# Kernel tuning notes

Measured on AMD Instinct MI355X. Metric: run time of the kernel, lower is better.

## Reference

```python
import jax, jax.numpy as jnp
import numpy as np

NUM_AUTHOR = 16604
NUM_PAPER = 12455
NUM_NODES = NUM_AUTHOR + NUM_PAPER  # 29059
EMBED_DIM = 300
B = 32768          # batch of query nodes
E = 1048576        # total neighbor edges (avg degree 32)


def setup_inputs() -> dict:
    key = jax.random.key(0)
    k1, k2, k3, k4, k5, k6 = jax.random.split(key, 6)
    nodes = jax.random.randint(k1, (B,), 0, NUM_NODES)
    seg = jnp.sort(jax.random.randint(k2, (E,), 0, B))
    neighbors = jax.random.randint(k3, (E,), 0, NUM_NODES)
    embeddings = jax.random.normal(k4, (NUM_NODES, EMBED_DIM), dtype=jnp.float32)
    # linear1: Linear(3*300 -> 300)
    lim = 1.0 / np.sqrt(3 * EMBED_DIM)
    W1 = jax.random.uniform(k5, (EMBED_DIM, 3 * EMBED_DIM), dtype=jnp.float32, minval=-lim, maxval=lim)
    b1 = jax.random.uniform(k6, (EMBED_DIM,), dtype=jnp.float32, minval=-lim, maxval=lim)
    return {"nodes": nodes, "seg": seg, "neighbors": neighbors,
            "embeddings": embeddings, "W1": W1, "b1": b1}


def reference(nodes, seg, neighbors, embeddings, W1, b1):
    # Gather neighbor embeddings: [E, D] (dominant memory traffic)
    nb_emb = embeddings[neighbors]
    # type_1 = same node type as the query node, type_2 = the other type
    same = (neighbors < NUM_AUTHOR) == (nodes[seg] < NUM_AUTHOR)  # [E] bool
    w1 = same.astype(nb_emb.dtype)[:, None]
    w2 = 1.0 - w1
    sum1 = jax.ops.segment_sum(nb_emb * w1, seg, num_segments=B)   # [B, D]
    sum2 = jax.ops.segment_sum(nb_emb * w2, seg, num_segments=B)
    cnt1 = jax.ops.segment_sum(w1[:, 0], seg, num_segments=B)[:, None]  # [B,1]
    cnt2 = jax.ops.segment_sum(w2[:, 0], seg, num_segments=B)[:, None]
    # mean pooling; empty type falls back to ones (as in the torch code)
    t1 = jnp.where(cnt1 > 0, sum1 / jnp.maximum(cnt1, 1.0), 1.0)
    t2 = jnp.where(cnt2 > 0, sum2 / jnp.maximum(cnt2, 1.0), 1.0)
    self_f = embeddings[nodes]  # [B, D]
    combined = jnp.concatenate([self_f, t1, t2], axis=-1)  # [B, 3D]
    return combined @ W1.T + b1  # [B, D]
```

## Files before the change

kernel.cpp:

```cpp
#include <hip/hip_runtime.h>
#include <hip/hip_bf16.h>

#define NUM_AUTHOR 16604
#define EMB_D      300
#define BQ         32768
#define NEDGE      1048576
#define KPAD 960
#define NPAD 320
#define DPAD 320
#define NNODES 29059

#define SEG_BLOCKS 4096
#define PW_BLOCKS  1200
#define CE_BLOCKS  4541

typedef __attribute__((ext_vector_type(8))) short bf16x8;
typedef __attribute__((ext_vector_type(4))) float f32x4;

__device__ __forceinline__ unsigned short f2bf(float f) {
  unsigned int u = __float_as_uint(f);
  u += 0x7fffu + ((u >> 16) & 1u);
  return (unsigned short)(u >> 16);
}

__device__ __forceinline__ void async_copy16(const void* g, void* lds_base) {
  __builtin_amdgcn_global_load_lds(
      (const __attribute__((address_space(1))) unsigned int*)g,
      (__attribute__((address_space(3))) unsigned int*)lds_base, 16, 0, 0);
}

__global__ void prep_all(const int* __restrict__ seg, int* __restrict__ start,
                         const float* __restrict__ W1, unsigned short* __restrict__ Wt,
                         const float* __restrict__ emb, unsigned short* __restrict__ embB) {
  int blk = blockIdx.x;
  if (blk < SEG_BLOCKS) {
    int i = blk * 256 + threadIdx.x;
    int s = seg[i];
    int prev = (i == 0) ? -1 : seg[i - 1];
    if (s != prev) {
      for (int b = prev + 1; b <= s; ++b) start[b] = i;
    }
    if (i == NEDGE - 1) {
      for (int b = s + 1; b <= BQ; ++b) start[b] = NEDGE;
    }
  } else if (blk < SEG_BLOCKS + PW_BLOCKS) {
    int i = (blk - SEG_BLOCKS) * 256 + threadIdx.x;
    int n = i / KPAD, k = i % KPAD;
    int sec = k / 320, kk = k % 320;
    unsigned short v = 0;
    if (n < 300 && kk < 300) v = f2bf(W1[n * 900 + sec * 300 + kk]);
    Wt[i] = v;
  } else {
    int i = (blk - SEG_BLOCKS - PW_BLOCKS) * 256 + threadIdx.x;
    if (i >= NNODES * 40) return;
    int r = i / 40, q = i % 40;
    const float* src = emb + (size_t)r * EMB_D + q * 8;
    unsigned int u[4] = {0, 0, 0, 0};
    if (q < 37) {
      float4 v0 = *(const float4*)src;
      float4 v1 = *(const float4*)(src + 4);
      u[0] = (unsigned int)f2bf(v0.x) | ((unsigned int)f2bf(v0.y) << 16);
      u[1] = (unsigned int)f2bf(v0.z) | ((unsigned int)f2bf(v0.w) << 16);
      u[2] = (unsigned int)f2bf(v1.x) | ((unsigned int)f2bf(v1.y) << 16);
      u[3] = (unsigned int)f2bf(v1.z) | ((unsigned int)f2bf(v1.w) << 16);
    } else if (q == 37) {
      float4 v0 = *(const float4*)src;
      u[0] = (unsigned int)f2bf(v0.x) | ((unsigned int)f2bf(v0.y) << 16);
      u[1] = (unsigned int)f2bf(v0.z) | ((unsigned int)f2bf(v0.w) << 16);
    }
    ((uint4*)embB)[i] = (uint4){u[0], u[1], u[2], u[3]};
  }
}

__device__ __forceinline__ void accum8(uint4 p, int bit,
                                       float2* atot, float2* a1) {
  unsigned int pk[4] = {p.x, p.y, p.z, p.w};
  float2 v[4];
  #pragma unroll
  for (int k = 0; k < 4; ++k) {
    v[k].x = __uint_as_float(pk[k] << 16);
    v[k].y = __uint_as_float(pk[k] & 0xffff0000u);
  }
  #pragma unroll
  for (int k = 0; k < 4; ++k) {
    atot[k].x += v[k].x; atot[k].y += v[k].y;
  }
  if (__builtin_amdgcn_readfirstlane(bit)) {
    #pragma unroll
    for (int k = 0; k < 4; ++k) {
      a1[k].x += v[k].x; a1[k].y += v[k].y;
    }
  }
}

__global__ __launch_bounds__(128) void pool(
    const int* __restrict__ nodes, const int* __restrict__ neighbors,
    const int* __restrict__ start, const unsigned short* __restrict__ embB,
    unsigned short* __restrict__ comb) {
  int b = blockIdx.x * 2 + (threadIdx.x >> 6);
  int l = threadIdx.x & 63;
  int s0 = start[b], s1 = start[b + 1];
  int node = nodes[b];
  int qa = (node < NUM_AUTHOR) ? 1 : 0;
  bool act = (l < 40);
  const unsigned short* ep = embB + 8 * l;

  float2 atot[4], a1[4];
  #pragma unroll
  for (int k = 0; k < 4; ++k) {
    atot[k] = make_float2(0.f, 0.f);
    a1[k]   = make_float2(0.f, 0.f);
  }
  int c1 = 0;
  int rem = s1 - s0;

  for (int base = 0; base < rem; base += 64) {
    int cl = min(64, rem - base);
    int idx = neighbors[s0 + base + min(l, cl - 1)];
    int same = (((idx < NUM_AUTHOR) ? 1 : 0) == qa) ? 1 : 0;
    unsigned long long bal = __ballot(same != 0);
    unsigned long long msk = (cl >= 64) ? ~0ull : ((1ull << cl) - 1ull);
    c1 += __popcll(bal & msk);
    int off = idx * DPAD;

    int j2 = 0;
    for (; j2 + 8 <= cl; j2 += 8) {
      int o[8];
      #pragma unroll
      for (int q = 0; q < 8; ++q) o[q] = __shfl(off, j2 + q);
      if (act) {
        uint4 p[8];
        #pragma unroll
        for (int q = 0; q < 8; ++q) p[q] = *(const uint4*)(ep + o[q]);
        #pragma unroll
        for (int q = 0; q < 8; ++q)
          accum8(p[q], (int)((bal >> (j2 + q)) & 1), atot, a1);
      }
    }
    for (; j2 < cl; ++j2) {
      int o = __shfl(off, j2);
      if (act) {
        uint4 p = *(const uint4*)(ep + o);
        accum8(p, (int)((bal >> j2) & 1), atot, a1);
      }
    }
  }

  int c2 = rem - c1;
  if (!act) return;

  uint4 selfv = *(const uint4*)(embB + (size_t)node * DPAD + 8 * l);
  float r1 = c1 ? 1.0f / (float)c1 : 0.0f;
  float r2 = c2 ? 1.0f / (float)c2 : 0.0f;
  unsigned int o1[4], o2[4];
  #pragma unroll
  for (int k = 0; k < 4; ++k) {
    float t1lo = c1 ? a1[k].x * r1 : 1.0f;
    float t1hi = c1 ? a1[k].y * r1 : 1.0f;
    float t2lo = c2 ? (atot[k].x - a1[k].x) * r2 : 1.0f;
    float t2hi = c2 ? (atot[k].y - a1[k].y) * r2 : 1.0f;
    o1[k] = (unsigned int)f2bf(t1lo) | ((unsigned int)f2bf(t1hi) << 16);
    o2[k] = (unsigned int)f2bf(t2lo) | ((unsigned int)f2bf(t2hi) << 16);
  }
  uint4* crow = (uint4*)(comb + (size_t)b * KPAD);
  crow[l]      = selfv;
  crow[40 + l] = (uint4){o1[0], o1[1], o1[2], o1[3]};
  crow[80 + l] = (uint4){o2[0], o2[1], o2[2], o2[3]};
}

__global__ __launch_bounds__(256) void gemm(
    const unsigned short* __restrict__ A,
    const unsigned short* __restrict__ Bt,
    const float* __restrict__ b1,
    float* __restrict__ out) {
  __shared__ __align__(16) unsigned short As[2][64 * 64];
  __shared__ __align__(16) unsigned short Bs[2][160 * 64];

  int tid  = threadIdx.x;
  int lane = tid & 63;
  int w    = tid >> 6;
  int quad = lane >> 4;
  int l16  = lane & 15;
  int bm = blockIdx.x >> 1;
  int bn = blockIdx.x & 1;
  int wm = w >> 1, wn = w & 1;

  f32x4 acc[2][5];
  for (int i = 0; i < 2; ++i)
    for (int j = 0; j < 5; ++j)
      acc[i][j] = (f32x4){0.f, 0.f, 0.f, 0.f};

  const size_t Abase = (size_t)bm * 64 * KPAD;
  const size_t Bbase = (size_t)bn * 160 * KPAD;

  auto stage = [&](int kt, int buf) {
    int k0 = kt * 64;
    for (int c = w; c < 8; c += 4) {
      int flat = c * 64 + lane;
      int row = flat >> 3, g = flat & 7;
      int kq = g ^ (row & 7);
      const unsigned short* gp = A + Abase + (size_t)row * KPAD + k0 + kq * 8;
      async_copy16(gp, (char*)&As[buf][0] + c * 1024);
    }
    for (int c = w; c < 20; c += 4) {
      int flat = c * 64 + lane;
      int row = flat >> 3, g = flat & 7;
      int kq = g ^ (row & 7);
      const unsigned short* gp = Bt + Bbase + (size_t)row * KPAD + k0 + kq * 8;
      async_copy16(gp, (char*)&Bs[buf][0] + c * 1024);
    }
  };

  stage(0, 0);
  for (int kt = 0; kt < KPAD / 64; ++kt) {
    int cur = kt & 1;
    __syncthreads();
    if (kt + 1 < KPAD / 64) stage(kt + 1, cur ^ 1);
    #pragma unroll
    for (int ks = 0; ks < 2; ++ks) {
      int gi = ks * 4 + quad;
      bf16x8 af[2], bf[5];
      #pragma unroll
      for (int rt = 0; rt < 2; ++rt) {
        int row = wm * 32 + rt * 16 + l16;
        af[rt] = *(const bf16x8*)&As[cur][row * 64 + ((gi ^ (row & 7)) << 3)];
      }
      #pragma unroll
      for (int ct = 0; ct < 5; ++ct) {
        int row = wn * 80 + ct * 16 + l16;
        bf[ct] = *(const bf16x8*)&Bs[cur][row * 64 + ((gi ^ (row & 7)) << 3)];
      }
      #pragma unroll
      for (int rt = 0; rt < 2; ++rt)
        #pragma unroll
        for (int ct = 0; ct < 5; ++ct)
          acc[rt][ct] = __builtin_amdgcn_mfma_f32_16x16x32_bf16(
              af[rt], bf[ct], acc[rt][ct], 0, 0, 0);
    }
  }

  int m0 = bm * 64 + wm * 32;
  int n0 = bn * 160 + wn * 80;
  for (int ct = 0; ct < 5; ++ct) {
    int n = n0 + ct * 16 + l16;
    if (n >= 300) continue;
    float bias = b1[n];
    for (int rt = 0; rt < 2; ++rt) {
      int m = m0 + rt * 16 + quad * 4;
      for (int r = 0; r < 4; ++r)
        out[(size_t)(m + r) * 300 + n] = acc[rt][ct][r] + bias;
    }
  }
}

__global__ __launch_bounds__(128) void pool_f32(
    const int* __restrict__ nodes, const int* __restrict__ neighbors,
    const int* __restrict__ start, const float* __restrict__ emb,
    unsigned short* __restrict__ comb) {
  int b = blockIdx.x;
  int t = threadIdx.x;
  if (t >= 80) return;
  int s0 = start[b], s1 = start[b + 1];
  int node = nodes[b];
  int qa = (node < NUM_AUTHOR) ? 1 : 0;
  bool act = (t < 75);
  float a1x = 0.f, a1y = 0.f, a1z = 0.f, a1w = 0.f;
  float a2x = 0.f, a2y = 0.f, a2z = 0.f, a2w = 0.f;
  int c1 = 0;
  #pragma unroll 2
  for (int j = s0; j < s1; ++j) {
    int nb = neighbors[j];
    int fl = (((nb < NUM_AUTHOR) ? 1 : 0) == qa) ? 1 : 0;
    c1 += fl;
    if (act) {
      const float4 v = *(const float4*)(emb + (size_t)nb * EMB_D + 4 * t);
      float w = fl ? 1.0f : 0.0f;
      float u = 1.0f - w;
      a1x += w * v.x; a1y += w * v.y; a1z += w * v.z; a1w += w * v.w;
      a2x += u * v.x; a2y += u * v.y; a2z += u * v.z; a2w += u * v.w;
    }
  }
  int c2 = (s1 - s0) - c1;
  unsigned int ps0 = 0, ps1 = 0, p10 = 0, p11 = 0, p20 = 0, p21 = 0;
  if (act) {
    const float4 sv = *(const float4*)(emb + (size_t)node * EMB_D + 4 * t);
    float r1 = c1 ? 1.0f / (float)c1 : 0.0f;
    float r2 = c2 ? 1.0f / (float)c2 : 0.0f;
    float t1x = c1 ? a1x * r1 : 1.0f, t1y = c1 ? a1y * r1 : 1.0f;
    float t1z = c1 ? a1z * r1 : 1.0f, t1w = c1 ? a1w * r1 : 1.0f;
    float t2x = c2 ? a2x * r2 : 1.0f, t2y = c2 ? a2y * r2 : 1.0f;
    float t2z = c2 ? a2z * r2 : 1.0f, t2w = c2 ? a2w * r2 : 1.0f;
    ps0 = (unsigned int)f2bf(sv.x) | ((unsigned int)f2bf(sv.y) << 16);
    ps1 = (unsigned int)f2bf(sv.z) | ((unsigned int)f2bf(sv.w) << 16);
    p10 = (unsigned int)f2bf(t1x) | ((unsigned int)f2bf(t1y) << 16);
    p11 = (unsigned int)f2bf(t1z) | ((unsigned int)f2bf(t1w) << 16);
    p20 = (unsigned int)f2bf(t2x) | ((unsigned int)f2bf(t2y) << 16);
    p21 = (unsigned int)f2bf(t2z) | ((unsigned int)f2bf(t2w) << 16);
  }
  unsigned int* crow = (unsigned int*)(comb + (size_t)b * KPAD);
  crow[2 * t]       = ps0;  crow[2 * t + 1]       = ps1;
  crow[160 + 2 * t] = p10;  crow[160 + 2 * t + 1] = p11;
  crow[320 + 2 * t] = p20;  crow[320 + 2 * t + 1] = p21;
}

__global__ void seg_bounds_only(const int* __restrict__ seg, int* __restrict__ start) {
  int i = blockIdx.x * 256 + threadIdx.x;
  if (i >= NEDGE) return;
  int s = seg[i];
  int prev = (i == 0) ? -1 : seg[i - 1];
  if (s != prev) for (int b = prev + 1; b <= s; ++b) start[b] = i;
  if (i == NEDGE - 1) for (int b = s + 1; b <= BQ; ++b) start[b] = NEDGE;
}
__global__ void prep_w_only(const float* __restrict__ W1, unsigned short* __restrict__ Wt) {
  int i = blockIdx.x * 256 + threadIdx.x;
  if (i >= NPAD * KPAD) return;
  int n = i / KPAD, k = i % KPAD;
  int sec = k / 320, kk = k % 320;
  unsigned short v = 0;
  if (n < 300 && kk < 300) v = f2bf(W1[n * 900 + sec * 300 + kk]);
  Wt[i] = v;
}

extern "C" void kernel_launch(void* const* d_in, const int* in_sizes, int n_in,
                              void* d_out, int out_size, void* d_ws, size_t ws_size,
                              hipStream_t stream) {
  const int* nodes     = (const int*)d_in[0];
  const int* seg       = (const int*)d_in[1];
  const int* neighbors = (const int*)d_in[2];
  const float* emb     = (const float*)d_in[3];
  const float* W1      = (const float*)d_in[4];
  const float* b1      = (const float*)d_in[5];
  float* out           = (float*)d_out;

  char* ws = (char*)d_ws;
  int* start           = (int*)ws;
  unsigned short* Wt   = (unsigned short*)(ws + 131584);
  unsigned short* comb = (unsigned short*)(ws + 746496);
  unsigned short* embB = (unsigned short*)(ws + 63661056);
  const size_t WS_NEEDED = 82258816;

  if (ws_size >= WS_NEEDED) {
    prep_all<<<SEG_BLOCKS + PW_BLOCKS + CE_BLOCKS, 256, 0, stream>>>(
        seg, start, W1, Wt, emb, embB);
    pool<<<BQ / 2, 128, 0, stream>>>(nodes, neighbors, start, embB, comb);
  } else {
    seg_bounds_only<<<SEG_BLOCKS, 256, 0, stream>>>(seg, start);
    prep_w_only<<<PW_BLOCKS, 256, 0, stream>>>(W1, Wt);
    pool_f32<<<BQ, 128, 0, stream>>>(nodes, neighbors, start, emb, comb);
  }
  gemm<<<1024, 256, 0, stream>>>(comb, Wt, b1, out);
}
```

Before: 227.2 us.

## Software-pipeline neighbor gathers in pool and enlarge GEMM tile to 128 rows

The pool kernel now reads neighbor indices straight from memory per lane, in groups of eight, and double-buffers the embedding gathers so the loads for the next group are issued while the current group is accumulated. This replaces the per-chunk ballot/shuffle scheme and adds an occupancy hint. The GEMM now uses a 128-row M tile in dynamic LDS with a swizzled block order for L2 locality, keeping the old kernel as a fallback. In exchange it uses more registers and more LDS per block, which lowers occupancy.

```diff
diff --git a/kernel.cpp b/kernel.cpp
--- a/kernel.cpp
+++ b/kernel.cpp
@@ -93,17 +93,20 @@
   }
 }
 
-__global__ __launch_bounds__(128) void pool(
+__global__ __launch_bounds__(128, 4) void pool(
     const int* __restrict__ nodes, const int* __restrict__ neighbors,
     const int* __restrict__ start, const unsigned short* __restrict__ embB,
     unsigned short* __restrict__ comb) {
   int b = blockIdx.x * 2 + (threadIdx.x >> 6);
   int l = threadIdx.x & 63;
-  int s0 = start[b], s1 = start[b + 1];
   int node = nodes[b];
   int qa = (node < NUM_AUTHOR) ? 1 : 0;
   bool act = (l < 40);
-  const unsigned short* ep = embB + 8 * l;
+
+  int s0u  = __builtin_amdgcn_readfirstlane(start[b]);
+  int remu = __builtin_amdgcn_readfirstlane(start[b + 1]) - s0u;
+  int qau  = __builtin_amdgcn_readfirstlane(qa);
+  const int* nb = neighbors + s0u;
 
   float2 atot[4], a1[4];
   #pragma unroll
@@ -112,41 +115,53 @@
     a1[k]   = make_float2(0.f, 0.f);
   }
   int c1 = 0;
-  int rem = s1 - s0;
-
-  for (int base = 0; base < rem; base += 64) {
-    int cl = min(64, rem - base);
-    int idx = neighbors[s0 + base + min(l, cl - 1)];
-    int same = (((idx < NUM_AUTHOR) ? 1 : 0) == qa) ? 1 : 0;
-    unsigned long long bal = __ballot(same != 0);
-    unsigned long long msk = (cl >= 64) ? ~0ull : ((1ull << cl) - 1ull);
-    c1 += __popcll(bal & msk);
-    int off = idx * DPAD;
-
-    int j2 = 0;
-    for (; j2 + 8 <= cl; j2 += 8) {
-      int o[8];
-      #pragma unroll
-      for (int q = 0; q < 8; ++q) o[q] = __shfl(off, j2 + q);
-      if (act) {
-        uint4 p[8];
-        #pragma unroll
-        for (int q = 0; q < 8; ++q) p[q] = *(const uint4*)(ep + o[q]);
-        #pragma unroll
-        for (int q = 0; q < 8; ++q)
-          accum8(p[q], (int)((bal >> (j2 + q)) & 1), atot, a1);
-      }
-    }
-    for (; j2 < cl; ++j2) {
-      int o = __shfl(off, j2);
-      if (act) {
-        uint4 p = *(const uint4*)(ep + o);
-        accum8(p, (int)((bal >> j2) & 1), atot, a1);
-      }
-    }
-  }
-
-  int c2 = rem - c1;
+
+  auto loadg = [&](uint4* p, int* bt, int g) {
+    #pragma unroll
+    for (int q = 0; q < 8; ++q) {
+      int ii = nb[g * 8 + q];
+      bt[q] = ((((ii < NUM_AUTHOR) ? 1 : 0) == qau) ? 1 : 0);
+      const unsigned short* rp = embB + (size_t)ii * DPAD;
+      if (act) p[q] = *(const uint4*)(rp + 8 * l);
+    }
+  };
+  auto accg = [&](const uint4* p, const int* bt) {
+    #pragma unroll
+    for (int q = 0; q < 8; ++q) {
+      c1 += bt[q];
+      if (act) accum8(p[q], bt[q], atot, a1);
+    }
+  };
+
+  int ng = remu >> 3;
+  if (ng > 0) {
+    uint4 pA[8], pB[8];
+    int bA[8], bB[8];
+    loadg(pA, bA, 0);
+    int g = 1;
+    for (; g + 1 < ng; g += 2) {
+      loadg(pB, bB, g);     accg(pA, bA);
+      loadg(pA, bA, g + 1); accg(pB, bB);
+    }
+    if (g < ng) {
+      loadg(pB, bB, g);     accg(pA, bA);
+      accg(pB, bB);
+    } else {
+      accg(pA, bA);
+    }
+  }
+  for (int j = ng * 8; j < remu; ++j) {
+    int ii = nb[j];
+    int bt = ((((ii < NUM_AUTHOR) ? 1 : 0) == qau) ? 1 : 0);
+    c1 += bt;
+    if (act) {
+      const unsigned short* rp = embB + (size_t)ii * DPAD;
+      uint4 p = *(const uint4*)(rp + 8 * l);
+      accum8(p, bt, atot, a1);
+    }
+  }
+
+  int c2 = remu - c1;
   if (!act) return;
 
   uint4 selfv = *(const uint4*)(embB + (size_t)node * DPAD + 8 * l);
@@ -173,6 +188,98 @@
     const unsigned short* __restrict__ Bt,
     const float* __restrict__ b1,
     float* __restrict__ out) {
+  extern __shared__ unsigned short lds[];
+  unsigned short* As = lds;
+  unsigned short* Bs = lds + 2 * 8192;
+
+  int tid  = threadIdx.x;
+  int lane = tid & 63;
+  int w    = tid >> 6;
+  int quad = lane >> 4;
+  int l16  = lane & 15;
+  int P = blockIdx.x;
+  int L = (P & 7) * 64 + (P >> 3);
+  int bm = L >> 1;
+  int bn = L & 1;
+  int wm = w >> 1, wn = w & 1;
+
+  f32x4 acc[4][5];
+  #pragma unroll
+  for (int i = 0; i < 4; ++i)
+    #pragma unroll
+    for (int j = 0; j < 5; ++j)
+      acc[i][j] = (f32x4){0.f, 0.f, 0.f, 0.f};
+
+  const size_t Abase = (size_t)bm * 128 * KPAD;
+  const size_t Bbase = (size_t)bn * 160 * KPAD;
+
+  auto stage = [&](int kt, int buf) {
+    int k0 = kt * 64;
+    char* Ad = (char*)(As + buf * 8192);
+    char* Bd = (char*)(Bs + buf * 10240);
+    for (int c = w; c < 16; c += 4) {
+      int flat = c * 64 + lane;
+      int row = flat >> 3, g = flat & 7;
+      int kq = g ^ (row & 7);
+      async_copy16(A + Abase + (size_t)row * KPAD + k0 + kq * 8, Ad + c * 1024);
+    }
+    for (int c = w; c < 20; c += 4) {
+      int flat = c * 64 + lane;
+      int row = flat >> 3, g = flat & 7;
+      int kq = g ^ (row & 7);
+      async_copy16(Bt + Bbase + (size_t)row * KPAD + k0 + kq * 8, Bd + c * 1024);
+    }
+  };
+
+  stage(0, 0);
+  for (int kt = 0; kt < KPAD / 64; ++kt) {
+    int cur = kt & 1;
+    __syncthreads();
+    if (kt + 1 < KPAD / 64) stage(kt + 1, cur ^ 1);
+    const unsigned short* Ac = As + cur * 8192;
+    const unsigned short* Bc = Bs + cur * 10240;
+    #pragma unroll
+    for (int ks = 0; ks < 2; ++ks) {
+      int gi = ks * 4 + quad;
+      bf16x8 af[4], bfr[5];
+      #pragma unroll
+      for (int rt = 0; rt < 4; ++rt) {
+        int row = wm * 64 + rt * 16 + l16;
+        af[rt] = *(const bf16x8*)&Ac[row * 64 + ((gi ^ (row & 7)) << 3)];
+      }
+      #pragma unroll
+      for (int ct = 0; ct < 5; ++ct) {
+        int row = wn * 80 + ct * 16 + l16;
+        bfr[ct] = *(const bf16x8*)&Bc[row * 64 + ((gi ^ (row & 7)) << 3)];
+      }
+      #pragma unroll
+      for (int rt = 0; rt < 4; ++rt)
+        #pragma unroll
+        for (int ct = 0; ct < 5; ++ct)
+          acc[rt][ct] = __builtin_amdgcn_mfma_f32_16x16x32_bf16(
+              af[rt], bfr[ct], acc[rt][ct], 0, 0, 0);
+    }
+  }
+
+  int m0 = bm * 128 + wm * 64;
+  int n0 = bn * 160 + wn * 80;
+  for (int ct = 0; ct < 5; ++ct) {
+    int n = n0 + ct * 16 + l16;
+    if (n >= 300) continue;
+    float bias = b1[n];
+    for (int rt = 0; rt < 4; ++rt) {
+      int m = m0 + rt * 16 + quad * 4;
+      for (int r = 0; r < 4; ++r)
+        out[(size_t)(m + r) * 300 + n] = acc[rt][ct][r] + bias;
+    }
+  }
+}
+
+__global__ __launch_bounds__(256) void gemm_fb(
+    const unsigned short* __restrict__ A,
+    const unsigned short* __restrict__ Bt,
+    const float* __restrict__ b1,
+    float* __restrict__ out) {
   __shared__ __align__(16) unsigned short As[2][64 * 64];
   __shared__ __align__(16) unsigned short Bs[2][160 * 64];
 
@@ -219,7 +326,7 @@
     #pragma unroll
     for (int ks = 0; ks < 2; ++ks) {
       int gi = ks * 4 + quad;
-      bf16x8 af[2], bf[5];
+      bf16x8 af[2], bfr[5];
       #pragma unroll
       for (int rt = 0; rt < 2; ++rt) {
         int row = wm * 32 + rt * 16 + l16;
@@ -228,14 +335,14 @@
       #pragma unroll
       for (int ct = 0; ct < 5; ++ct) {
         int row = wn * 80 + ct * 16 + l16;
-        bf[ct] = *(const bf16x8*)&Bs[cur][row * 64 + ((gi ^ (row & 7)) << 3)];
+        bfr[ct] = *(const bf16x8*)&Bs[cur][row * 64 + ((gi ^ (row & 7)) << 3)];
       }
       #pragma unroll
       for (int rt = 0; rt < 2; ++rt)
         #pragma unroll
         for (int ct = 0; ct < 5; ++ct)
           acc[rt][ct] = __builtin_amdgcn_mfma_f32_16x16x32_bf16(
-              af[rt], bf[ct], acc[rt][ct], 0, 0, 0);
+              af[rt], bfr[ct], acc[rt][ct], 0, 0, 0);
     }
   }
 
@@ -339,6 +446,14 @@
   unsigned short* embB = (unsigned short*)(ws + 63661056);
   const size_t WS_NEEDED = 82258816;
 
+  static int big_lds_ok = -1;
+  if (big_lds_ok < 0) {
+    big_lds_ok = (hipFuncSetAttribute(
+                      reinterpret_cast<const void*>(gemm),
+                      hipFuncAttributeMaxDynamicSharedMemorySize,
+                      73728) == hipSuccess) ? 1 : 0;
+  }
+
   if (ws_size >= WS_NEEDED) {
     prep_all<<<SEG_BLOCKS + PW_BLOCKS + CE_BLOCKS, 256, 0, stream>>>(
         seg, start, W1, Wt, emb, embB);
@@ -348,5 +463,9 @@
     prep_w_only<<<PW_BLOCKS, 256, 0, stream>>>(W1, Wt);
     pool_f32<<<BQ, 128, 0, stream>>>(nodes, neighbors, start, emb, comb);
   }
-  gemm<<<1024, 256, 0, stream>>>(comb, Wt, b1, out);
-}
+  if (big_lds_ok) {
+    gemm<<<512, 256, 73728, stream>>>(comb, Wt, b1, out);
+  } else {
+    gemm_fb<<<1024, 256, 0, stream>>>(comb, Wt, b1, out);
+  }
+}
```

Result: slower. 352.6 us (+55.2%).
